# Kernel tuning notes

Measured on AMD Instinct MI355X. Metric: run time of the kernel, lower is better.

## Reference

```python
import jax, jax.numpy as jnp
import numpy as np

B, CIN, H, W = 32, 64, 128, 128
HID, OUT, E, S, R = 64, 64, 8, 2, 16
TOP_K = 2
TEMP = 2.0
BN_EPS = 1e-5


def setup_inputs() -> dict:
    key = jax.random.key(0)
    ks = jax.random.split(key, 16)
    sc = lambda fan: 1.0 / np.sqrt(fan)
    h2 = 2 * HID
    return {
        "x": jax.random.normal(ks[0], (B, CIN, H, W), jnp.float32),
        "fe_w": jax.random.normal(ks[1], (HID, CIN), jnp.float32) * sc(CIN),
        "fe_b": jnp.zeros((HID,), jnp.float32),
        "s_w": jax.random.normal(ks[2], (S, OUT, HID), jnp.float32) * sc(HID),
        "s_b": jnp.zeros((S, OUT), jnp.float32),
        "e_w": jax.random.normal(ks[3], (E, OUT, HID), jnp.float32) * sc(HID),
        "e_b": jnp.zeros((E, OUT), jnp.float32),
        "g1_w": jax.random.normal(ks[4], (h2, HID), jnp.float32) * sc(HID),
        "g1_b": jnp.zeros((h2,), jnp.float32),
        "bn1_g": jnp.ones((h2,), jnp.float32),
        "bn1_b": jnp.zeros((h2,), jnp.float32),
        "ca1_w": jax.random.normal(ks[5], (h2 // R, h2), jnp.float32) * sc(h2),
        "ca1_b": jnp.zeros((h2 // R,), jnp.float32),
        "ca2_w": jax.random.normal(ks[6], (h2, h2 // R), jnp.float32) * sc(h2 // R),
        "ca2_b": jnp.zeros((h2,), jnp.float32),
        "g2_w": jax.random.normal(ks[7], (HID, h2), jnp.float32) * sc(h2),
        "g2_b": jnp.zeros((HID,), jnp.float32),
        "bn2_g": jnp.ones((HID,), jnp.float32),
        "bn2_b": jnp.zeros((HID,), jnp.float32),
        "g3_w": jax.random.normal(ks[8], (E, HID), jnp.float32) * sc(HID),
        "g3_b": jnp.zeros((E,), jnp.float32),
    }


def _gelu(v):
    return jax.nn.gelu(v, approximate=False)


def _bn_eval(v, g, b):
    # BatchNorm eval mode with running_mean=0, running_var=1
    return v * (g / np.sqrt(1.0 + BN_EPS)) + b


def reference(x, fe_w, fe_b, s_w, s_b, e_w, e_b, g1_w, g1_b, bn1_g, bn1_b,
              ca1_w, ca1_b, ca2_w, ca2_b, g2_w, g2_b, bn2_g, bn2_b, g3_w, g3_b):
    # feature extractor: 1x1 conv + GELU
    features = _gelu(jnp.einsum('bchw,oc->bohw', x, fe_w) + fe_b[None, :, None, None])

    # shared experts: mean of S expert outputs (sum / S)
    shared = _gelu(jnp.einsum('bchw,soc->bsohw', features, s_w)
                   + s_b[None, :, :, None, None]).mean(axis=1)

    # gating on globally pooled features [B, HID]
    gf = features.mean(axis=(2, 3))
    h1 = _gelu(_bn_eval(gf @ g1_w.T + g1_b, bn1_g, bn1_b))  # [B, 2*HID]
    # ChannelAttention on 1x1 spatial: avg_pool == max_pool == identity
    att = _gelu(h1 @ ca1_w.T + ca1_b) @ ca2_w.T + ca2_b
    h1 = h1 * jax.nn.sigmoid(att + att)  # avg_out + max_out are identical
    hh = _gelu(_bn_eval(h1 @ g2_w.T + g2_b, bn2_g, bn2_b))  # [B, HID]
    scores = hh @ g3_w.T + g3_b  # [B, E]

    top_vals, top_idx = jax.lax.top_k(scores, TOP_K)
    top_w = jax.nn.softmax(top_vals / TEMP, axis=1)  # [B, TOP_K]
    # dense per-(sample, expert) weights
    dense_w = jnp.zeros((x.shape[0], E), scores.dtype).at[
        jnp.arange(x.shape[0])[:, None], top_idx].add(top_w)

    # all experts on full batch, then weighted accumulate (matches original loop)
    eo = _gelu(jnp.einsum('bchw,eoc->beohw', features, e_w)
               + e_b[None, :, :, None, None])  # [B, E, OUT, H, W]
    routed = jnp.einsum('beohw,be->bohw', eo, dense_w)

    return shared + routed
```

## Files before the change

### kernel.cpp

```cpp
#include <hip/hip_runtime.h>
#include <hip/hip_bf16.h>
#include <stdint.h>

#define HW 16384

typedef __bf16 bf16_t;
typedef bf16_t bf16x8 __attribute__((ext_vector_type(8)));
typedef float f32x4 __attribute__((ext_vector_type(4)));

__device__ __forceinline__ float gelu_f(float x) {
    float t = x * fmaf(x * x, 0.044715f, 1.0f);
    float e = __builtin_amdgcn_exp2f(-2.3022083f * t);
    return x * __builtin_amdgcn_rcpf(1.0f + e);
}

__device__ __forceinline__ uint32_t pk2(float a, float b) {
    union { bf16_t h[2]; uint32_t u; } z;
    z.h[0] = (bf16_t)a; z.h[1] = (bf16_t)b;
    return z.u;
}

__device__ __forceinline__ void load16_to_lds(const float* g, float* lds) {
    __builtin_amdgcn_global_load_lds(
        (const __attribute__((address_space(1))) uint32_t*)g,
        (__attribute__((address_space(3))) uint32_t*)lds, 16, 0, 0);
}

__device__ __forceinline__ bf16x8 frag8(const float* src) {
    float4 lo = ((const float4*)src)[0];
    float4 hi = ((const float4*)src)[1];
    bf16x8 r;
    r[0] = (bf16_t)lo.x; r[1] = (bf16_t)lo.y; r[2] = (bf16_t)lo.z; r[3] = (bf16_t)lo.w;
    r[4] = (bf16_t)hi.x; r[5] = (bf16_t)hi.y; r[6] = (bf16_t)hi.z; r[7] = (bf16_t)hi.w;
    return r;
}

__global__ __launch_bounds__(256, 4)
void k1_feat(const float* __restrict__ x, const float* __restrict__ fe_w,
             const float* __restrict__ fe_b, bf16_t* __restrict__ feat,
             float* __restrict__ gf_part) {
    __shared__ float xs[2][64 * 64];
    __shared__ float gf4[4][64];

    int tid = threadIdx.x;
    int lane = tid & 63;
    int wid = tid >> 6;
    int r16 = lane & 15;
    int g = lane >> 4;
    int b = blockIdx.x >> 5;
    int ss = blockIdx.x & 31;
    int p0 = ss * 512;

    bf16x8 A[4][2];
    f32x4 bias[4];
#pragma unroll
    for (int ot = 0; ot < 4; ++ot) {
#pragma unroll
        for (int kh = 0; kh < 2; ++kh)
            A[ot][kh] = frag8(fe_w + (ot * 16 + r16) * 64 + kh * 32 + g * 8);
#pragma unroll
        for (int r = 0; r < 4; ++r) bias[ot][r] = fe_b[ot * 16 + g * 4 + r];
    }

    int j16 = lane & 15;
    int rsub = lane >> 4;

    auto STAGE = [&](int buf, int i) {
#pragma unroll
        for (int s = 0; s < 4; ++s) {
            int c0 = wid * 16 + s * 4;
            int c = c0 + rsub;
            int gch = j16 ^ (((c >> 3) & 3) << 2);
            const float* gsrc = x + (size_t)(b * 64 + c) * HW + p0 + i * 64 + gch * 4;
            load16_to_lds(gsrc, &xs[buf][c0 * 64]);
        }
    };

    float gfp[4][4] = {};
    bf16_t* featb = feat + (size_t)b * HW * 64;
    int wb = 16 * (wid ^ g) + r16;

    auto COMPUTE = [&](int buf, int i) {
        bf16x8 B0, B1;
#pragma unroll
        for (int j = 0; j < 8; ++j) {
            B0[j] = (bf16_t)xs[buf][(g * 8 + j) * 64 + wb];
            B1[j] = (bf16_t)xs[buf][(32 + g * 8 + j) * 64 + wb];
        }
        int pg = p0 + i * 64 + wid * 16 + r16;
#pragma unroll
        for (int ot = 0; ot < 4; ++ot) {
            f32x4 y = {0.f, 0.f, 0.f, 0.f};
            y = __builtin_amdgcn_mfma_f32_16x16x32_bf16(A[ot][0], B0, y, 0, 0, 0);
            y = __builtin_amdgcn_mfma_f32_16x16x32_bf16(A[ot][1], B1, y, 0, 0, 0);
            float vr[4];
#pragma unroll
            for (int r = 0; r < 4; ++r) {
                float v = gelu_f(y[r] + bias[ot][r]);
                gfp[ot][r] += v;
                vr[r] = v;
            }
            uint2 st;
            st.x = pk2(vr[0], vr[1]);
            st.y = pk2(vr[2], vr[3]);
            *(uint2*)(featb + (size_t)pg * 64 + ot * 16 + g * 4) = st;
        }
    };

    STAGE(0, 0);
    STAGE(1, 1);
    asm volatile("s_waitcnt vmcnt(4)" ::: "memory");
    __builtin_amdgcn_s_barrier();

#pragma unroll
    for (int i = 0; i < 8; ++i) {
        COMPUTE(i & 1, i);
        asm volatile("s_waitcnt lgkmcnt(0)" ::: "memory");
        __builtin_amdgcn_s_barrier();
        if (i < 6) {
            STAGE(i & 1, i + 2);
            asm volatile("s_waitcnt vmcnt(8)" ::: "memory");
            __builtin_amdgcn_s_barrier();
        } else if (i == 6) {
            asm volatile("s_waitcnt vmcnt(4)" ::: "memory");
            __builtin_amdgcn_s_barrier();
        }
    }

#pragma unroll
    for (int ot = 0; ot < 4; ++ot)
#pragma unroll
        for (int r = 0; r < 4; ++r) {
            float v = gfp[ot][r];
            v += __shfl_xor(v, 1);
            v += __shfl_xor(v, 2);
            v += __shfl_xor(v, 4);
            v += __shfl_xor(v, 8);
            if (r16 == 0) gf4[wid][ot * 16 + g * 4 + r] = v;
        }
    __syncthreads();
    if (tid < 64)
        gf_part[(size_t)blockIdx.x * 64 + tid] =
            gf4[0][tid] + gf4[1][tid] + gf4[2][tid] + gf4[3][tid];
}

__global__ __launch_bounds__(256)
void k2_gate(const float* __restrict__ gf_part,
             const float* __restrict__ g1_w, const float* __restrict__ g1_b,
             const float* __restrict__ bn1_g, const float* __restrict__ bn1_b,
             const float* __restrict__ ca1_w, const float* __restrict__ ca1_b,
             const float* __restrict__ ca2_w, const float* __restrict__ ca2_b,
             const float* __restrict__ g2_w, const float* __restrict__ g2_b,
             const float* __restrict__ bn2_g, const float* __restrict__ bn2_b,
             const float* __restrict__ g3_w, const float* __restrict__ g3_b,
             int* __restrict__ gidx, float* __restrict__ gw) {
    __shared__ float w1t[128 * 65];
    __shared__ float wc1[8 * 129];
    __shared__ float wc2[128 * 9];
    __shared__ float w2t[64 * 129];
    __shared__ float w3[8 * 65];
    __shared__ float gf[64], h1[128], a1[8], hh[64], sc[8];
    const float R1 = 0.99999500003749969f;
    int tid = threadIdx.x;
    int b = blockIdx.x;

    for (int i = tid; i < 2048; i += 256) {
        float4 v = ((const float4*)g1_w)[i];
        float* d = w1t + (i >> 4) * 65 + (i & 15) * 4;
        d[0] = v.x; d[1] = v.y; d[2] = v.z; d[3] = v.w;
    }
    for (int i = tid; i < 2048; i += 256) {
        float4 v = ((const float4*)g2_w)[i];
        float* d = w2t + (i >> 5) * 129 + (i & 31) * 4;
        d[0] = v.x; d[1] = v.y; d[2] = v.z; d[3] = v.w;
    }
    if (tid < 256) {
        int i = tid;
        float4 v = ((const float4*)ca1_w)[i];
        float* d = wc1 + (i >> 5) * 129 + (i & 31) * 4;
        d[0] = v.x; d[1] = v.y; d[2] = v.z; d[3] = v.w;
    }
    if (tid < 256) {
        int i = tid;
        float4 v = ((const float4*)ca2_w)[i];
        float* d = wc2 + (i >> 1) * 9 + (i & 1) * 4;
        d[0] = v.x; d[1] = v.y; d[2] = v.z; d[3] = v.w;
    }
    if (tid < 128) {
        int i = tid;
        float4 v = ((const float4*)g3_w)[i];
        float* d = w3 + (i >> 4) * 65 + (i & 15) * 4;
        d[0] = v.x; d[1] = v.y; d[2] = v.z; d[3] = v.w;
    }
    if (tid < 64) {
        float s0 = 0.f, s1 = 0.f;
#pragma unroll
        for (int ssi = 0; ssi < 32; ssi += 2) {
            s0 += gf_part[(size_t)(b * 32 + ssi) * 64 + tid];
            s1 += gf_part[(size_t)(b * 32 + ssi + 1) * 64 + tid];
        }
        gf[tid] = (s0 + s1) * (1.0f / 16384.0f);
    }
    __syncthreads();

    if (tid < 128) {
        int j = tid;
        float s0 = 0.f, s1 = 0.f;
#pragma unroll 8
        for (int c = 0; c < 64; c += 2) {
            s0 += gf[c] * w1t[j * 65 + c];
            s1 += gf[c + 1] * w1t[j * 65 + c + 1];
        }
        float s = g1_b[j] + s0 + s1;
        s = s * (bn1_g[j] * R1) + bn1_b[j];
        h1[j] = gelu_f(s);
    }
    __syncthreads();
    if (tid < 8) {
        int j = tid;
        float s0 = 0.f, s1 = 0.f;
#pragma unroll 8
        for (int c = 0; c < 128; c += 2) {
            s0 += h1[c] * wc1[j * 129 + c];
            s1 += h1[c + 1] * wc1[j * 129 + c + 1];
        }
        a1[j] = gelu_f(ca1_b[j] + s0 + s1);
    }
    __syncthreads();
    if (tid < 128) {
        int j = tid;
        float s = ca2_b[j];
#pragma unroll
        for (int r = 0; r < 8; ++r) s += a1[r] * wc2[j * 9 + r];
        float e2 = __builtin_amdgcn_exp2f(-2.8853901f * s);
        h1[j] = h1[j] * __builtin_amdgcn_rcpf(1.0f + e2);
    }
    __syncthreads();
    if (tid < 64) {
        int j = tid;
        float s0 = 0.f, s1 = 0.f;
#pragma unroll 8
        for (int c = 0; c < 128; c += 2) {
            s0 += h1[c] * w2t[j * 129 + c];
            s1 += h1[c + 1] * w2t[j * 129 + c + 1];
        }
        float s = g2_b[j] + s0 + s1;
        s = s * (bn2_g[j] * R1) + bn2_b[j];
        hh[j] = gelu_f(s);
    }
    __syncthreads();
    if (tid < 8) {
        int j = tid;
        float s0 = 0.f, s1 = 0.f;
#pragma unroll 8
        for (int c = 0; c < 64; c += 2) {
            s0 += hh[c] * w3[j * 65 + c];
            s1 += hh[c + 1] * w3[j * 65 + c + 1];
        }
        sc[j] = g3_b[j] + s0 + s1;
    }
    __syncthreads();
    if (tid == 0) {
        float v0 = -1e30f, v1 = -1e30f;
        int i0 = 0, i1 = 0;
#pragma unroll
        for (int e = 0; e < 8; ++e) {
            float s = sc[e];
            if (s > v0) { v1 = v0; i1 = i0; v0 = s; i0 = e; }
            else if (s > v1) { v1 = s; i1 = e; }
        }
        float t = __builtin_amdgcn_exp2f(0.7213475f * (v1 - v0));
        float den = __builtin_amdgcn_rcpf(1.0f + t);
        gidx[b * 2] = i0; gidx[b * 2 + 1] = i1;
        gw[b * 2] = den; gw[b * 2 + 1] = t * den;
    }
}

__global__ __launch_bounds__(256, 4)
void k3_out(const bf16_t* __restrict__ feat, const float* __restrict__ s_w,
            const float* __restrict__ s_b, const float* __restrict__ e_w,
            const float* __restrict__ e_b, const int* __restrict__ gidx,
            const float* __restrict__ gw, float* __restrict__ out) {
    int tid = threadIdx.x;
    int lane = tid & 63, wid = tid >> 6;
    int r16 = lane & 15, g = lane >> 4;
    int b = blockIdx.x >> 5;
    int stripe = blockIdx.x & 31;

    int i0 = gidx[2 * b], i1 = gidx[2 * b + 1];
    float coef[4] = {0.5f, 0.5f, gw[2 * b], gw[2 * b + 1]};
    const float* Wm[4] = {s_w, s_w + 4096,
                          e_w + (size_t)i0 * 4096, e_w + (size_t)i1 * 4096};
    const float* Bv[4] = {s_b, s_b + 64, e_b + i0 * 64, e_b + i1 * 64};

    bf16x8 Wf[4][2];
    float bias[4];
    int row = wid * 16 + r16;
#pragma unroll
    for (int m = 0; m < 4; ++m) {
#pragma unroll
        for (int kh = 0; kh < 2; ++kh)
            Wf[m][kh] = frag8(Wm[m] + row * 64 + kh * 32 + g * 8);
        bias[m] = Bv[m][row];
    }

    const uint4* fb = (const uint4*)(feat + (size_t)b * HW * 64);
    float* outb = out + ((size_t)b * 64 + row) * HW + stripe * 512;
    int pbase = stripe * 512 + r16;

    auto BODY = [&](int t, uint4 u0, uint4 u1) {
        bf16x8 F0 = __builtin_bit_cast(bf16x8, u0);
        bf16x8 F1 = __builtin_bit_cast(bf16x8, u1);
        f32x4 acc = {0.f, 0.f, 0.f, 0.f};
#pragma unroll
        for (int m = 0; m < 4; ++m) {
            f32x4 y = {0.f, 0.f, 0.f, 0.f};
            y = __builtin_amdgcn_mfma_f32_16x16x32_bf16(F0, Wf[m][0], y, 0, 0, 0);
            y = __builtin_amdgcn_mfma_f32_16x16x32_bf16(F1, Wf[m][1], y, 0, 0, 0);
#pragma unroll
            for (int r = 0; r < 4; ++r)
                acc[r] += coef[m] * gelu_f(y[r] + bias[m]);
        }
        float4 st = {acc[0], acc[1], acc[2], acc[3]};
        *(float4*)(outb + t * 16 + g * 4) = st;
    };

    uint4 u0 = fb[(size_t)pbase * 8 + g];
    uint4 u1 = fb[(size_t)pbase * 8 + 4 + g];
#pragma unroll 4
    for (int t = 0; t < 31; ++t) {
        uint4 n0 = fb[(size_t)(pbase + (t + 1) * 16) * 8 + g];
        uint4 n1 = fb[(size_t)(pbase + (t + 1) * 16) * 8 + 4 + g];
        BODY(t, u0, u1);
        u0 = n0; u1 = n1;
    }
    BODY(31, u0, u1);
}

extern "C" void kernel_launch(void* const* d_in, const int* in_sizes, int n_in,
                              void* d_out, int out_size, void* d_ws, size_t ws_size,
                              hipStream_t stream) {
    (void)in_sizes; (void)n_in; (void)out_size; (void)ws_size;
    const float* x     = (const float*)d_in[0];
    const float* fe_w  = (const float*)d_in[1];
    const float* fe_b  = (const float*)d_in[2];
    const float* s_w   = (const float*)d_in[3];
    const float* s_b   = (const float*)d_in[4];
    const float* e_w   = (const float*)d_in[5];
    const float* e_b   = (const float*)d_in[6];
    const float* g1_w  = (const float*)d_in[7];
    const float* g1_b  = (const float*)d_in[8];
    const float* bn1_g = (const float*)d_in[9];
    const float* bn1_b = (const float*)d_in[10];
    const float* ca1_w = (const float*)d_in[11];
    const float* ca1_b = (const float*)d_in[12];
    const float* ca2_w = (const float*)d_in[13];
    const float* ca2_b = (const float*)d_in[14];
    const float* g2_w  = (const float*)d_in[15];
    const float* g2_b  = (const float*)d_in[16];
    const float* bn2_g = (const float*)d_in[17];
    const float* bn2_b = (const float*)d_in[18];
    const float* g3_w  = (const float*)d_in[19];
    const float* g3_b  = (const float*)d_in[20];
    float* out = (float*)d_out;

    char* wsb = (char*)d_ws;
    bf16_t* feat   = (bf16_t*)wsb;
    float* gf_part = (float*)(wsb + 67108864);
    int* gidx      = (int*)(wsb + 67108864 + 262144);
    float* gwts    = (float*)(wsb + 67108864 + 262144 + 256);

    k1_feat<<<1024, 256, 0, stream>>>(x, fe_w, fe_b, feat, gf_part);
    k2_gate<<<32, 256, 0, stream>>>(gf_part, g1_w, g1_b, bn1_g, bn1_b, ca1_w, ca1_b,
                                    ca2_w, ca2_b, g2_w, g2_b, bn2_g, bn2_b, g3_w, g3_b,
                                    gidx, gwts);
    k3_out<<<1024, 256, 0, stream>>>(feat, s_w, s_b, e_w, e_b, gidx, gwts, out);
}
```

Measured before the change: 388.5 us.

## Triple-buffer feature kernel staging and widen feature stores via channel permutation

```diff
diff --git a/kernel.cpp b/kernel.cpp
--- a/kernel.cpp
+++ b/kernel.cpp
@@ -35,11 +35,20 @@
     return r;
 }
 
-__global__ __launch_bounds__(256, 4)
+__device__ __forceinline__ bf16x8 frag44(const float* a, const float* b) {
+    float4 lo = *(const float4*)a;
+    float4 hi = *(const float4*)b;
+    bf16x8 r;
+    r[0] = (bf16_t)lo.x; r[1] = (bf16_t)lo.y; r[2] = (bf16_t)lo.z; r[3] = (bf16_t)lo.w;
+    r[4] = (bf16_t)hi.x; r[5] = (bf16_t)hi.y; r[6] = (bf16_t)hi.z; r[7] = (bf16_t)hi.w;
+    return r;
+}
+
+__global__ __launch_bounds__(256, 3)
 void k1_feat(const float* __restrict__ x, const float* __restrict__ fe_w,
              const float* __restrict__ fe_b, bf16_t* __restrict__ feat,
              float* __restrict__ gf_part) {
-    __shared__ float xs[2][64 * 64];
+    __shared__ float xs[3][64 * 64];
     __shared__ float gf4[4][64];
 
     int tid = threadIdx.x;
@@ -61,6 +70,7 @@
 #pragma unroll
         for (int r = 0; r < 4; ++r) bias[ot][r] = fe_b[ot * 16 + g * 4 + r];
     }
+    asm volatile("" ::: "memory");
 
     int j16 = lane & 15;
     int rsub = lane >> 4;
@@ -88,44 +98,50 @@
             B1[j] = (bf16_t)xs[buf][(32 + g * 8 + j) * 64 + wb];
         }
         int pg = p0 + i * 64 + wid * 16 + r16;
+        float vals[4][4];
 #pragma unroll
         for (int ot = 0; ot < 4; ++ot) {
             f32x4 y = {0.f, 0.f, 0.f, 0.f};
             y = __builtin_amdgcn_mfma_f32_16x16x32_bf16(A[ot][0], B0, y, 0, 0, 0);
             y = __builtin_amdgcn_mfma_f32_16x16x32_bf16(A[ot][1], B1, y, 0, 0, 0);
-            float vr[4];
 #pragma unroll
             for (int r = 0; r < 4; ++r) {
                 float v = gelu_f(y[r] + bias[ot][r]);
                 gfp[ot][r] += v;
-                vr[r] = v;
+                vals[ot][r] = v;
             }
-            uint2 st;
-            st.x = pk2(vr[0], vr[1]);
-            st.y = pk2(vr[2], vr[3]);
-            *(uint2*)(featb + (size_t)pg * 64 + ot * 16 + g * 4) = st;
-        }
+        }
+        uint4 lo, hi;
+        lo.x = pk2(vals[0][0], vals[0][1]); lo.y = pk2(vals[0][2], vals[0][3]);
+        lo.z = pk2(vals[1][0], vals[1][1]); lo.w = pk2(vals[1][2], vals[1][3]);
+        hi.x = pk2(vals[2][0], vals[2][1]); hi.y = pk2(vals[2][2], vals[2][3]);
+        hi.z = pk2(vals[3][0], vals[3][1]); hi.w = pk2(vals[3][2], vals[3][3]);
+        uint4* dst = (uint4*)(featb + (size_t)pg * 64 + g * 16);
+        dst[0] = lo;
+        dst[1] = hi;
     };
 
-    STAGE(0, 0);
-    STAGE(1, 1);
-    asm volatile("s_waitcnt vmcnt(4)" ::: "memory");
+    STAGE(0, 0); STAGE(1, 1); STAGE(2, 2);
+    asm volatile("s_waitcnt vmcnt(8)" ::: "memory");
     __builtin_amdgcn_s_barrier();
 
-#pragma unroll
-    for (int i = 0; i < 8; ++i) {
-        COMPUTE(i & 1, i);
-        asm volatile("s_waitcnt lgkmcnt(0)" ::: "memory");
-        __builtin_amdgcn_s_barrier();
-        if (i < 6) {
-            STAGE(i & 1, i + 2);
-            asm volatile("s_waitcnt vmcnt(8)" ::: "memory");
-            __builtin_amdgcn_s_barrier();
-        } else if (i == 6) {
-            asm volatile("s_waitcnt vmcnt(4)" ::: "memory");
-            __builtin_amdgcn_s_barrier();
-        }
-    }
+#define K1_STEP(i, buf, VM, ...) \
+    COMPUTE(buf, i); \
+    asm volatile("s_waitcnt lgkmcnt(0)" ::: "memory"); \
+    __builtin_amdgcn_s_barrier(); \
+    __VA_ARGS__; \
+    asm volatile("s_waitcnt " VM ::: "memory"); \
+    __builtin_amdgcn_s_barrier();
+
+    K1_STEP(0, 0, "vmcnt(10)", STAGE(0, 3))
+    K1_STEP(1, 1, "vmcnt(12)", STAGE(1, 4))
+    K1_STEP(2, 2, "vmcnt(12)", STAGE(2, 5))
+    K1_STEP(3, 0, "vmcnt(12)", STAGE(0, 6))
+    K1_STEP(4, 1, "vmcnt(12)", STAGE(1, 7))
+    K1_STEP(5, 2, "vmcnt(8)")
+    K1_STEP(6, 0, "vmcnt(4)")
+    COMPUTE(1, 7);
+#undef K1_STEP
 
 #pragma unroll
     for (int ot = 0; ot < 4; ++ot)
@@ -299,8 +315,11 @@
 #pragma unroll
     for (int m = 0; m < 4; ++m) {
 #pragma unroll
-        for (int kh = 0; kh < 2; ++kh)
-            Wf[m][kh] = frag8(Wm[m] + row * 64 + kh * 32 + g * 8);
+        for (int kh = 0; kh < 2; ++kh) {
+            int base = (g & 1) * 32 + (kh * 2 + (g >> 1)) * 4;
+            Wf[m][kh] = frag44(Wm[m] + row * 64 + base,
+                               Wm[m] + row * 64 + base + 16);
+        }
         bias[m] = Bv[m][row];
     }
 
```

Measured after the change: 359.0 us. -7.6%, faster.
